# Optimization experiments

Measured on AMD Instinct MI355X. Metric: run time of the kernel, lower is better.

## Reference

```python
import jax, jax.numpy as jnp
import numpy as np

N = 50000   # nodes
E = 800000  # edges
F = 128     # num_node_features
H = 256     # hidden_channels
C = 40      # num_classes


def setup_inputs() -> dict:
    key = jax.random.key(0)
    ks = jax.random.split(key, 8)
    x = jax.random.normal(ks[0], (N, F), dtype=jnp.float32)
    edge_index = jax.random.randint(ks[1], (2, E), 0, N, dtype=jnp.int32)
    # GCNConv linear weights (PyG: lin has no bias; bias added post-aggregation)
    W1 = jax.random.normal(ks[2], (H, F), dtype=jnp.float32) * (1.0 / np.sqrt(F))
    b1 = jnp.zeros((H,), dtype=jnp.float32)
    W2 = jax.random.normal(ks[3], (H, H), dtype=jnp.float32) * (1.0 / np.sqrt(H))
    b2 = jnp.zeros((H,), dtype=jnp.float32)
    Wout = jax.random.normal(ks[4], (C, H), dtype=jnp.float32) * (1.0 / np.sqrt(H))
    bout = jnp.zeros((C,), dtype=jnp.float32)
    return {"x": x, "edge_index": edge_index,
            "W1": W1, "b1": b1, "W2": W2, "b2": b2,
            "Wout": Wout, "bout": bout}


def gcn_conv(x, src, dst, W, b, n):
    """PyG GCNConv: sym-normalized aggregation with self-loops.
    deg computed as in-degree on dst (gcn_norm), +1 for self loop.
    """
    h = x @ W.T  # [n, out]
    ones = jnp.ones((src.shape[0],), dtype=h.dtype)
    deg = jax.ops.segment_sum(ones, dst, num_segments=n) + 1.0  # self loop
    dinv = jax.lax.rsqrt(deg)  # deg >= 1, safe
    norm = dinv[src] * dinv[dst]                 # [E]
    agg = jax.ops.segment_sum(norm[:, None] * h[src], dst, num_segments=n)
    agg = agg + (dinv * dinv)[:, None] * h       # self-loop term
    return agg + b


def reference(x, edge_index, W1, b1, W2, b2, Wout, bout):
    src, dst = edge_index[0], edge_index[1]
    h = jax.nn.relu(gcn_conv(x, src, dst, W1, b1, N))
    h = gcn_conv(h, src, dst, W2, b2, N)
    return h @ Wout.T + bout  # [N, C] logits
```

## Files before the change

### kernel.cpp

```cpp
#include <hip/hip_runtime.h>

#define N_NODES 50000
#define N_EDGES 800000
#define F_IN    128
#define H_DIM   256
#define C_OUT   40
#define MT_TOT  (N_NODES / 16)
#define TPAD    64
#define NBIN1   196
#define NCHB    200
#define CHSZ    (N_EDGES / NCHB)

typedef unsigned short u16;
typedef unsigned int   u32;
typedef short bf16x8 __attribute__((ext_vector_type(8)));
typedef float f32x4  __attribute__((ext_vector_type(4)));

__device__ inline float bfbits2f(u16 u) { return __uint_as_float(((u32)u) << 16); }
__device__ inline u16 f2bf(float f) {
    u32 u = __float_as_uint(f);
    u += 0x7fffu + ((u >> 16) & 1u);
    return (u16)(u >> 16);
}
__device__ inline u32 pack2(float a, float b) {
    return (u32)f2bf(a) | ((u32)f2bf(b) << 16);
}

#define CVT_X  (N_NODES * F_IN / 4)
#define CVT_W1 (H_DIM * F_IN / 4)
#define CVT_TOT (CVT_X + CVT_W1)
#define CC_CVT_BLKS (CVT_TOT / 256)
__global__ __launch_bounds__(256) void cvtwc_k(const float4* __restrict__ x, uint2* __restrict__ xb,
                                               const float4* __restrict__ W1, uint2* __restrict__ W1b,
                                               const float* __restrict__ W2, const float* __restrict__ Wo,
                                               const float* __restrict__ b2, const float* __restrict__ bo,
                                               u16* __restrict__ Wcb, float* __restrict__ bc) {
    if (blockIdx.x < CC_CVT_BLKS) {
        int i = blockIdx.x * 256 + threadIdx.x;
        const float4* s; uint2* d; int j;
        if (i < CVT_X) { s = x; d = xb; j = i; }
        else { s = W1; d = W1b; j = i - CVT_X; }
        float4 v = s[j];
        uint2 o; o.x = pack2(v.x, v.y); o.y = pack2(v.z, v.w);
        d[j] = o;
        return;
    }
    const int c = blockIdx.x - CC_CVT_BLKS;
    const int t = threadIdx.x;
    float acc = 0.f;
    for (int o = 0; o < H_DIM; o += 8) {
        float w2v[8];
#pragma unroll
        for (int j = 0; j < 8; j++) w2v[j] = W2[(size_t)(o + j) * H_DIM + t];
#pragma unroll
        for (int j = 0; j < 8; j++) acc += Wo[(size_t)c * H_DIM + o + j] * w2v[j];
    }
    Wcb[(size_t)c * H_DIM + t] = f2bf(acc);
    __shared__ float red[256];
    red[t] = b2[t] * Wo[(size_t)c * H_DIM + t];
    __syncthreads();
    for (int off = 128; off > 0; off >>= 1) {
        if (t < off) red[t] += red[t + off];
        __syncthreads();
    }
    if (t == 0) bc[c] = red[0] + bo[c];
}

__global__ __launch_bounds__(256) void p1hist_k(const int* __restrict__ dst, int* __restrict__ Ht) {
    __shared__ int hist[NBIN1];
    const int t = threadIdx.x;
    const int b = blockIdx.x;
    if (t < NBIN1) hist[t] = 0;
    __syncthreads();
    for (int i = b * CHSZ + t; i < (b + 1) * CHSZ; i += 256)
        atomicAdd(&hist[dst[i] >> 8], 1);
    __syncthreads();
    if (t < NBIN1) Ht[t * NCHB + b] = hist[t];
}

__global__ __launch_bounds__(256) void p1scan_k(int* __restrict__ Ht, int* __restrict__ totals) {
    __shared__ int sc[256];
    const int t = threadIdx.x;
    const int g = blockIdx.x;
    int v = (t < NCHB) ? Ht[g * NCHB + t] : 0;
    sc[t] = v;
    __syncthreads();
    for (int off = 1; off < 256; off <<= 1) {
        int u = (t >= off) ? sc[t - off] : 0;
        __syncthreads();
        sc[t] += u;
        __syncthreads();
    }
    if (t < NCHB) Ht[g * NCHB + t] = sc[t] - v;
    if (t == NCHB - 1) totals[g] = sc[t];
}

__global__ __launch_bounds__(256) void p1base_k(const int* __restrict__ totals,
                                                int* __restrict__ base, int* __restrict__ rowptr) {
    __shared__ int sc[256];
    const int t = threadIdx.x;
    int v = (t < NBIN1) ? totals[t] : 0;
    sc[t] = v;
    __syncthreads();
    for (int off = 1; off < 256; off <<= 1) {
        int u = (t >= off) ? sc[t - off] : 0;
        __syncthreads();
        sc[t] += u;
        __syncthreads();
    }
    if (t < NBIN1) base[t] = sc[t] - v;
    if (t == NBIN1 - 1) base[NBIN1] = sc[t];
    if (t == 0) rowptr[N_NODES] = N_EDGES;
}

__global__ __launch_bounds__(256) void p2scatter_k(const int* __restrict__ src, const int* __restrict__ dst,
                                                   const int* __restrict__ Ht, const int* __restrict__ base,
                                                   uint2* __restrict__ T) {
    __shared__ int cur[NBIN1];
    const int t = threadIdx.x;
    const int b = blockIdx.x;
    if (t < NBIN1) cur[t] = base[t] + Ht[t * NCHB + b];
    __syncthreads();
    for (int i = b * CHSZ + t; i < (b + 1) * CHSZ; i += 256) {
        const int s = src[i], d = dst[i];
        const int pos = atomicAdd(&cur[d >> 8], 1);
        uint2 ed; ed.x = (u32)s; ed.y = (u32)d;
        T[pos] = ed;
    }
}

__global__ __launch_bounds__(256) void p3a_k(const uint2* __restrict__ T, const int* __restrict__ base,
                                             int* __restrict__ rowptr, float* __restrict__ dinv) {
    __shared__ int hcnt[256];
    __shared__ int sc[256];
    const int t = threadIdx.x;
    const int g = blockIdx.x;
    const int nbeg = base[g], nend = base[g + 1];
    hcnt[t] = 0;
    __syncthreads();
    for (int i = nbeg + t; i < nend; i += 256)
        atomicAdd(&hcnt[T[i].y & 255], 1);
    __syncthreads();
    const int my = hcnt[t];
    sc[t] = my;
    __syncthreads();
    for (int off = 1; off < 256; off <<= 1) {
        int u = (t >= off) ? sc[t - off] : 0;
        __syncthreads();
        sc[t] += u;
        __syncthreads();
    }
    const int node = g * 256 + t;
    if (node < N_NODES) {
        rowptr[node] = nbeg + sc[t] - my;
        dinv[node] = rsqrtf((float)my + 1.0f);
    }
}

__global__ __launch_bounds__(256) void p3b_k(const uint2* __restrict__ T, const int* __restrict__ base,
                                             const float* __restrict__ dinv, uint2* __restrict__ edata) {
    __shared__ int hcnt[256];
    __shared__ int sc[256];
    __shared__ int cur[256];
    const int t = threadIdx.x;
    const int g = blockIdx.x;
    const int nbeg = base[g], nend = base[g + 1];
    hcnt[t] = 0;
    __syncthreads();
    for (int i = nbeg + t; i < nend; i += 256)
        atomicAdd(&hcnt[T[i].y & 255], 1);
    __syncthreads();
    const int my = hcnt[t];
    sc[t] = my;
    __syncthreads();
    for (int off = 1; off < 256; off <<= 1) {
        int u = (t >= off) ? sc[t - off] : 0;
        __syncthreads();
        sc[t] += u;
        __syncthreads();
    }
    cur[t] = nbeg + sc[t] - my;
    __syncthreads();
    for (int i = nbeg + t; i < nend; i += 256) {
        const uint2 e = T[i];
        const int pos = atomicAdd(&cur[e.y & 255], 1);
        const float w = dinv[e.x];
        uint2 ed; ed.x = e.x; ed.y = __float_as_uint(w);
        edata[pos] = ed;
    }
}

__global__ __launch_bounds__(256) void gather1_k(const u32* __restrict__ xb,
                                                 const int* __restrict__ rowptr,
                                                 const uint2* __restrict__ edata,
                                                 const float* __restrict__ dinv,
                                                 u32* __restrict__ aggx) {
    const int node = __builtin_amdgcn_readfirstlane(blockIdx.x * 4 + (threadIdx.x >> 6));
    const int lane = threadIdx.x & 63;
    if (node >= N_NODES) return;
    const int beg = __builtin_amdgcn_readfirstlane(rowptr[node]);
    const int end = __builtin_amdgcn_readfirstlane(rowptr[node + 1]);
    const float dd = dinv[node];
    const u32 vs = xb[(size_t)node * 64 + lane];
    float a0 = dd * bfbits2f((u16)vs);
    float a1 = dd * bfbits2f((u16)(vs >> 16));
    int e = beg;
    for (; e + 7 < end; e += 8) {
        uint2 ed[8];
#pragma unroll
        for (int j = 0; j < 8; j++) ed[j] = edata[e + j];
        u32 v[8];
#pragma unroll
        for (int j = 0; j < 8; j++) v[j] = xb[(size_t)ed[j].x * 64 + lane];
#pragma unroll
        for (int j = 0; j < 8; j++) {
            const float n = __uint_as_float(ed[j].y);
            a0 += n * bfbits2f((u16)v[j]);
            a1 += n * bfbits2f((u16)(v[j] >> 16));
        }
    }
    for (; e < end; e++) {
        const uint2 e0 = edata[e];
        const u32 v0 = xb[(size_t)e0.x * 64 + lane];
        const float n0 = __uint_as_float(e0.y);
        a0 += n0 * bfbits2f((u16)v0);
        a1 += n0 * bfbits2f((u16)(v0 >> 16));
    }
    aggx[(size_t)node * 64 + lane] = pack2(dd * a0, dd * a1);
}

__global__ __launch_bounds__(256) void bgemm1f_k(const u16* __restrict__ X,
                                                 const u16* __restrict__ W1b,
                                                 const float* __restrict__ b1,
                                                 const u16* __restrict__ Wcb,
                                                 u16* __restrict__ tb) {
    constexpr int KF1 = F_IN / 32;
    constexpr int KF2 = H_DIM / 32;
    __shared__ __align__(16) u16 hs[2][16][H_DIM + 8];
    const int wave = threadIdx.x >> 6;
    const int lane = threadIdx.x & 63;
    const int quad = lane >> 4;
    const int nn = lane & 15;
    const int ngbase = wave * 64;

    bf16x8 Bf[4][KF1];
    float bb[4];
#pragma unroll
    for (int j = 0; j < 4; j++) {
        const int wr = ngbase + j * 16 + nn;
#pragma unroll
        for (int kf = 0; kf < KF1; kf++)
            Bf[j][kf] = *(const bf16x8*)(W1b + (size_t)wr * F_IN + kf * 32 + quad * 8);
        bb[j] = b1[wr];
    }
    bf16x8 Bh[KF2];
    {
        int hr = wave * 16 + nn;
        if (hr > C_OUT - 1) hr = C_OUT - 1;
#pragma unroll
        for (int kf = 0; kf < KF2; kf++)
            Bh[kf] = *(const bf16x8*)(Wcb + (size_t)hr * H_DIM + kf * 32 + quad * 8);
    }

    int mt = blockIdx.x;
    if (mt >= MT_TOT) return;
    const int stride = gridDim.x;
    int buf = 0;

    bf16x8 Acur[KF1], Anext[KF1];
    {
        const u16* ap = X + (size_t)(mt * 16 + nn) * F_IN + quad * 8;
#pragma unroll
        for (int kf = 0; kf < KF1; kf++) Acur[kf] = *(const bf16x8*)(ap + kf * 32);
    }

    while (true) {
        const int mtn = mt + stride;
        if (mtn < MT_TOT) {
            const u16* ap = X + (size_t)(mtn * 16 + nn) * F_IN + quad * 8;
#pragma unroll
            for (int kf = 0; kf < KF1; kf++) Anext[kf] = *(const bf16x8*)(ap + kf * 32);
        }

        f32x4 acc[4];
#pragma unroll
        for (int j = 0; j < 4; j++) acc[j] = (f32x4){0.f, 0.f, 0.f, 0.f};
#pragma unroll
        for (int kf = 0; kf < KF1; kf++)
#pragma unroll
            for (int j = 0; j < 4; j++)
                acc[j] = __builtin_amdgcn_mfma_f32_16x16x32_bf16(Acur[kf], Bf[j][kf], acc[j], 0, 0, 0);

#pragma unroll
        for (int j = 0; j < 4; j++)
#pragma unroll
            for (int r = 0; r < 4; r++)
                hs[buf][quad * 4 + r][ngbase + j * 16 + nn] = f2bf(fmaxf(acc[j][r] + bb[j], 0.f));
        __syncthreads();

        if (wave < 3) {
            f32x4 ah = (f32x4){0.f, 0.f, 0.f, 0.f};
#pragma unroll
            for (int kf = 0; kf < KF2; kf++) {
                bf16x8 af = *(const bf16x8*)(&hs[buf][nn][kf * 32 + quad * 8]);
                ah = __builtin_amdgcn_mfma_f32_16x16x32_bf16(af, Bh[kf], ah, 0, 0, 0);
            }
            const int col = wave * 16 + nn;
#pragma unroll
            for (int r = 0; r < 4; r++) {
                const int row = mt * 16 + quad * 4 + r;
                tb[(size_t)row * TPAD + col] = f2bf(ah[r]);
            }
        }

        if (mtn >= MT_TOT) break;
#pragma unroll
        for (int kf = 0; kf < KF1; kf++) Acur[kf] = Anext[kf];
        mt = mtn;
        buf ^= 1;
    }
}

__global__ __launch_bounds__(256) void gatherO_k(const u32* __restrict__ tb,
                                                 const int* __restrict__ rowptr,
                                                 const uint2* __restrict__ edata,
                                                 const float* __restrict__ dinv,
                                                 const float* __restrict__ bc,
                                                 float* __restrict__ out) {
    const int node = __builtin_amdgcn_readfirstlane(blockIdx.x * 4 + (threadIdx.x >> 6));
    const int lane = threadIdx.x & 63;
    if (node >= N_NODES) return;
    const int lc = lane & 31;
    const int beg = __builtin_amdgcn_readfirstlane(rowptr[node]);
    const int end = __builtin_amdgcn_readfirstlane(rowptr[node + 1]);
    const float dd = dinv[node];
    const u32 vs = tb[(size_t)node * (TPAD / 2) + lc];
    float a0 = dd * bfbits2f((u16)vs);
    float a1 = dd * bfbits2f((u16)(vs >> 16));
    int e = beg;
    for (; e + 7 < end; e += 8) {
        uint2 ed[8];
#pragma unroll
        for (int j = 0; j < 8; j++) ed[j] = edata[e + j];
        u32 v[8];
#pragma unroll
        for (int j = 0; j < 8; j++) v[j] = tb[(size_t)ed[j].x * (TPAD / 2) + lc];
#pragma unroll
        for (int j = 0; j < 8; j++) {
            const float n = __uint_as_float(ed[j].y);
            a0 += n * bfbits2f((u16)v[j]);
            a1 += n * bfbits2f((u16)(v[j] >> 16));
        }
    }
    for (; e < end; e++) {
        const uint2 e0 = edata[e];
        const u32 v0 = tb[(size_t)e0.x * (TPAD / 2) + lc];
        const float n0 = __uint_as_float(e0.y);
        a0 += n0 * bfbits2f((u16)v0);
        a1 += n0 * bfbits2f((u16)(v0 >> 16));
    }
    if (lane < C_OUT / 2) {
        float2 o;
        o.x = dd * a0 + bc[2 * lane];
        o.y = dd * a1 + bc[2 * lane + 1];
        *(float2*)(out + (size_t)node * C_OUT + 2 * lane) = o;
    }
}

extern "C" void kernel_launch(void* const* d_in, const int* in_sizes, int n_in,
                              void* d_out, int out_size, void* d_ws, size_t ws_size,
                              hipStream_t stream) {
    const float* x    = (const float*)d_in[0];
    const int*   ei   = (const int*)d_in[1];
    const float* W1   = (const float*)d_in[2];
    const float* b1   = (const float*)d_in[3];
    const float* W2   = (const float*)d_in[4];
    const float* b2   = (const float*)d_in[5];
    const float* Wout = (const float*)d_in[6];
    const float* bout = (const float*)d_in[7];
    float* out = (float*)d_out;

    const int* src = ei;
    const int* dst = ei + N_EDGES;

    char* ws = (char*)d_ws;
    size_t o = 0;
    auto alloc = [&](size_t bytes) { size_t p = o; o = (o + bytes + 255) & ~(size_t)255; return p; };
    int*   Ht     = (int*)(ws + alloc((size_t)NBIN1 * NCHB * 4));
    int*   totals = (int*)(ws + alloc((size_t)NBIN1 * 4));
    int*   base   = (int*)(ws + alloc((size_t)(NBIN1 + 1) * 4));
    float* dinv   = (float*)(ws + alloc((size_t)N_NODES * 4));
    int*   rowptr = (int*)(ws + alloc((size_t)(N_NODES + 1) * 4));
    uint2* T      = (uint2*)(ws + alloc((size_t)N_EDGES * 8));
    uint2* edata  = (uint2*)(ws + alloc((size_t)N_EDGES * 8));
    u16*   xb     = (u16*)(ws + alloc((size_t)N_NODES * F_IN * 2));
    u16*   aggxb  = (u16*)(ws + alloc((size_t)N_NODES * F_IN * 2));
    u16*   tb     = (u16*)(ws + alloc((size_t)N_NODES * TPAD * 2));
    u16*   W1b    = (u16*)(ws + alloc((size_t)H_DIM * F_IN * 2));
    u16*   Wcb    = (u16*)(ws + alloc((size_t)C_OUT * H_DIM * 2));
    float* bc     = (float*)(ws + alloc((size_t)C_OUT * 4));

    cvtwc_k<<<CC_CVT_BLKS + C_OUT, 256, 0, stream>>>(
        (const float4*)x, (uint2*)xb, (const float4*)W1, (uint2*)W1b,
        W2, Wout, b2, bout, Wcb, bc);

    p1hist_k<<<NCHB, 256, 0, stream>>>(dst, Ht);
    p1scan_k<<<NBIN1, 256, 0, stream>>>(Ht, totals);
    p1base_k<<<1, 256, 0, stream>>>(totals, base, rowptr);
    p2scatter_k<<<NCHB, 256, 0, stream>>>(src, dst, Ht, base, T);
    p3a_k<<<NBIN1, 256, 0, stream>>>(T, base, rowptr, dinv);
    p3b_k<<<NBIN1, 256, 0, stream>>>(T, base, dinv, edata);

    gather1_k<<<(N_NODES + 3) / 4, 256, 0, stream>>>((const u32*)xb, rowptr, edata, dinv, (u32*)aggxb);
    bgemm1f_k<<<768, 256, 0, stream>>>(aggxb, W1b, b1, Wcb, tb);
    gatherO_k<<<(N_NODES + 3) / 4, 256, 0, stream>>>((const u32*)tb, rowptr, edata, dinv, bc, out);
}
```

Baseline: 206.1 us.

## Fold source-side degree scaling into features, shrink edge data to indices

Pre-scales x rows by dinv during the bf16 conversion and scales the layer-2 projected features by dinv in the GEMM epilogue. The per-edge norm weight is then no longer needed, so edata shrinks from (src, weight) pairs to plain src indices. This lets the two CSR build passes merge into one kernel, and the histogram is fused with the weight precompute. The aim is to cut edge-stream bandwidth in both gathers and to drop one kernel launch, in exchange for an extra pass that reads dinv while converting x.

New measurement: 199.7 us. 3.1% less time.

```diff
diff --git a/kernel.cpp b/kernel.cpp
--- a/kernel.cpp
+++ b/kernel.cpp
@@ -10,6 +10,8 @@
 #define NBIN1   196
 #define NCHB    200
 #define CHSZ    (N_EDGES / NCHB)
+#define CVT_X   (N_NODES * F_IN / 4)
+#define CVT_W1B (H_DIM * F_IN / 4 / 256)
 
 typedef unsigned short u16;
 typedef unsigned int   u32;
@@ -26,27 +28,32 @@
     return (u32)f2bf(a) | ((u32)f2bf(b) << 16);
 }
 
-#define CVT_X  (N_NODES * F_IN / 4)
-#define CVT_W1 (H_DIM * F_IN / 4)
-#define CVT_TOT (CVT_X + CVT_W1)
-#define CC_CVT_BLKS (CVT_TOT / 256)
-__global__ __launch_bounds__(256) void cvtwc_k(const float4* __restrict__ x, uint2* __restrict__ xb,
-                                               const float4* __restrict__ W1, uint2* __restrict__ W1b,
-                                               const float* __restrict__ W2, const float* __restrict__ Wo,
-                                               const float* __restrict__ b2, const float* __restrict__ bo,
-                                               u16* __restrict__ Wcb, float* __restrict__ bc) {
-    if (blockIdx.x < CC_CVT_BLKS) {
-        int i = blockIdx.x * 256 + threadIdx.x;
-        const float4* s; uint2* d; int j;
-        if (i < CVT_X) { s = x; d = xb; j = i; }
-        else { s = W1; d = W1b; j = i - CVT_X; }
-        float4 v = s[j];
+__global__ __launch_bounds__(256) void pre_k(const int* __restrict__ dst, int* __restrict__ Ht,
+                                             const float4* __restrict__ W1, uint2* __restrict__ W1b,
+                                             const float* __restrict__ W2, const float* __restrict__ Wo,
+                                             const float* __restrict__ b2, const float* __restrict__ bo,
+                                             u16* __restrict__ Wcb, float* __restrict__ bc) {
+    __shared__ int hist[NBIN1];
+    __shared__ float red[256];
+    const int t = threadIdx.x;
+    if (blockIdx.x < NCHB) {
+        const int b = blockIdx.x;
+        if (t < NBIN1) hist[t] = 0;
+        __syncthreads();
+        for (int i = b * CHSZ + t; i < (b + 1) * CHSZ; i += 256)
+            atomicAdd(&hist[dst[i] >> 8], 1);
+        __syncthreads();
+        if (t < NBIN1) Ht[t * NCHB + b] = hist[t];
+        return;
+    }
+    if (blockIdx.x < NCHB + CVT_W1B) {
+        int i = (blockIdx.x - NCHB) * 256 + t;
+        float4 v = W1[i];
         uint2 o; o.x = pack2(v.x, v.y); o.y = pack2(v.z, v.w);
-        d[j] = o;
+        W1b[i] = o;
         return;
     }
-    const int c = blockIdx.x - CC_CVT_BLKS;
-    const int t = threadIdx.x;
+    const int c = blockIdx.x - NCHB - CVT_W1B;
     float acc = 0.f;
     for (int o = 0; o < H_DIM; o += 8) {
         float w2v[8];
@@ -56,7 +63,6 @@
         for (int j = 0; j < 8; j++) acc += Wo[(size_t)c * H_DIM + o + j] * w2v[j];
     }
     Wcb[(size_t)c * H_DIM + t] = f2bf(acc);
-    __shared__ float red[256];
     red[t] = b2[t] * Wo[(size_t)c * H_DIM + t];
     __syncthreads();
     for (int off = 128; off > 0; off >>= 1) {
@@ -64,18 +70,6 @@
         __syncthreads();
     }
     if (t == 0) bc[c] = red[0] + bo[c];
-}
-
-__global__ __launch_bounds__(256) void p1hist_k(const int* __restrict__ dst, int* __restrict__ Ht) {
-    __shared__ int hist[NBIN1];
-    const int t = threadIdx.x;
-    const int b = blockIdx.x;
-    if (t < NBIN1) hist[t] = 0;
-    __syncthreads();
-    for (int i = b * CHSZ + t; i < (b + 1) * CHSZ; i += 256)
-        atomicAdd(&hist[dst[i] >> 8], 1);
-    __syncthreads();
-    if (t < NBIN1) Ht[t * NCHB + b] = hist[t];
 }
 
 __global__ __launch_bounds__(256) void p1scan_k(int* __restrict__ Ht, int* __restrict__ totals) {
@@ -129,10 +123,12 @@
     }
 }
 
-__global__ __launch_bounds__(256) void p3a_k(const uint2* __restrict__ T, const int* __restrict__ base,
-                                             int* __restrict__ rowptr, float* __restrict__ dinv) {
+__global__ __launch_bounds__(256) void p3_k(const uint2* __restrict__ T, const int* __restrict__ base,
+                                            int* __restrict__ rowptr, float* __restrict__ dinv,
+                                            u32* __restrict__ edata) {
     __shared__ int hcnt[256];
     __shared__ int sc[256];
+    __shared__ int cur[256];
     const int t = threadIdx.x;
     const int g = blockIdx.x;
     const int nbeg = base[g], nend = base[g + 1];
@@ -150,49 +146,36 @@
         sc[t] += u;
         __syncthreads();
     }
+    const int rbeg = nbeg + sc[t] - my;
     const int node = g * 256 + t;
     if (node < N_NODES) {
-        rowptr[node] = nbeg + sc[t] - my;
+        rowptr[node] = rbeg;
         dinv[node] = rsqrtf((float)my + 1.0f);
     }
-}
-
-__global__ __launch_bounds__(256) void p3b_k(const uint2* __restrict__ T, const int* __restrict__ base,
-                                             const float* __restrict__ dinv, uint2* __restrict__ edata) {
-    __shared__ int hcnt[256];
-    __shared__ int sc[256];
-    __shared__ int cur[256];
-    const int t = threadIdx.x;
-    const int g = blockIdx.x;
-    const int nbeg = base[g], nend = base[g + 1];
-    hcnt[t] = 0;
-    __syncthreads();
-    for (int i = nbeg + t; i < nend; i += 256)
-        atomicAdd(&hcnt[T[i].y & 255], 1);
-    __syncthreads();
-    const int my = hcnt[t];
-    sc[t] = my;
-    __syncthreads();
-    for (int off = 1; off < 256; off <<= 1) {
-        int u = (t >= off) ? sc[t - off] : 0;
-        __syncthreads();
-        sc[t] += u;
-        __syncthreads();
-    }
-    cur[t] = nbeg + sc[t] - my;
+    cur[t] = rbeg;
     __syncthreads();
     for (int i = nbeg + t; i < nend; i += 256) {
         const uint2 e = T[i];
         const int pos = atomicAdd(&cur[e.y & 255], 1);
-        const float w = dinv[e.x];
-        uint2 ed; ed.x = e.x; ed.y = __float_as_uint(w);
-        edata[pos] = ed;
-    }
+        edata[pos] = e.x;
+    }
+}
+
+__global__ __launch_bounds__(256) void xcvt_k(const float4* __restrict__ x,
+                                              const float* __restrict__ dinv,
+                                              uint2* __restrict__ xb) {
+    int i = blockIdx.x * 256 + threadIdx.x;
+    if (i >= CVT_X) return;
+    const int row = i >> 5;
+    const float s = dinv[row];
+    float4 v = x[i];
+    uint2 o; o.x = pack2(s * v.x, s * v.y); o.y = pack2(s * v.z, s * v.w);
+    xb[i] = o;
 }
 
 __global__ __launch_bounds__(256) void gather1_k(const u32* __restrict__ xb,
                                                  const int* __restrict__ rowptr,
-                                                 const uint2* __restrict__ edata,
+                                                 const u32* __restrict__ edata,
                                                  const float* __restrict__ dinv,
                                                  u32* __restrict__ aggx) {
     const int node = __builtin_amdgcn_readfirstlane(blockIdx.x * 4 + (threadIdx.x >> 6));
@@ -202,29 +185,26 @@
     const int end = __builtin_amdgcn_readfirstlane(rowptr[node + 1]);
     const float dd = dinv[node];
     const u32 vs = xb[(size_t)node * 64 + lane];
-    float a0 = dd * bfbits2f((u16)vs);
-    float a1 = dd * bfbits2f((u16)(vs >> 16));
+    float a0 = bfbits2f((u16)vs);
+    float a1 = bfbits2f((u16)(vs >> 16));
     int e = beg;
     for (; e + 7 < end; e += 8) {
-        uint2 ed[8];
-#pragma unroll
-        for (int j = 0; j < 8; j++) ed[j] = edata[e + j];
+        u32 s8[8];
+#pragma unroll
+        for (int j = 0; j < 8; j++) s8[j] = edata[e + j];
         u32 v[8];
 #pragma unroll
-        for (int j = 0; j < 8; j++) v[j] = xb[(size_t)ed[j].x * 64 + lane];
+        for (int j = 0; j < 8; j++) v[j] = xb[(size_t)s8[j] * 64 + lane];
 #pragma unroll
         for (int j = 0; j < 8; j++) {
-            const float n = __uint_as_float(ed[j].y);
-            a0 += n * bfbits2f((u16)v[j]);
-            a1 += n * bfbits2f((u16)(v[j] >> 16));
+            a0 += bfbits2f((u16)v[j]);
+            a1 += bfbits2f((u16)(v[j] >> 16));
         }
     }
     for (; e < end; e++) {
-        const uint2 e0 = edata[e];
-        const u32 v0 = xb[(size_t)e0.x * 64 + lane];
-        const float n0 = __uint_as_float(e0.y);
-        a0 += n0 * bfbits2f((u16)v0);
-        a1 += n0 * bfbits2f((u16)(v0 >> 16));
+        const u32 v0 = xb[(size_t)edata[e] * 64 + lane];
+        a0 += bfbits2f((u16)v0);
+        a1 += bfbits2f((u16)(v0 >> 16));
     }
     aggx[(size_t)node * 64 + lane] = pack2(dd * a0, dd * a1);
 }
@@ -233,6 +213,7 @@
                                                  const u16* __restrict__ W1b,
                                                  const float* __restrict__ b1,
                                                  const u16* __restrict__ Wcb,
+                                                 const float* __restrict__ dinv,
                                                  u16* __restrict__ tb) {
     constexpr int KF1 = F_IN / 32;
     constexpr int KF2 = H_DIM / 32;
@@ -309,7 +290,7 @@
 #pragma unroll
             for (int r = 0; r < 4; r++) {
                 const int row = mt * 16 + quad * 4 + r;
-                tb[(size_t)row * TPAD + col] = f2bf(ah[r]);
+                tb[(size_t)row * TPAD + col] = f2bf(dinv[row] * ah[r]);
             }
         }
 
@@ -323,7 +304,7 @@
 
 __global__ __launch_bounds__(256) void gatherO_k(const u32* __restrict__ tb,
                                                  const int* __restrict__ rowptr,
-                                                 const uint2* __restrict__ edata,
+                                                 const u32* __restrict__ edata,
                                                  const float* __restrict__ dinv,
                                                  const float* __restrict__ bc,
                                                  float* __restrict__ out) {
@@ -335,29 +316,26 @@
     const int end = __builtin_amdgcn_readfirstlane(rowptr[node + 1]);
     const float dd = dinv[node];
     const u32 vs = tb[(size_t)node * (TPAD / 2) + lc];
-    float a0 = dd * bfbits2f((u16)vs);
-    float a1 = dd * bfbits2f((u16)(vs >> 16));
+    float a0 = bfbits2f((u16)vs);
+    float a1 = bfbits2f((u16)(vs >> 16));
     int e = beg;
     for (; e + 7 < end; e += 8) {
-        uint2 ed[8];
-#pragma unroll
-        for (int j = 0; j < 8; j++) ed[j] = edata[e + j];
+        u32 s8[8];
+#pragma unroll
+        for (int j = 0; j < 8; j++) s8[j] = edata[e + j];
         u32 v[8];
 #pragma unroll
-        for (int j = 0; j < 8; j++) v[j] = tb[(size_t)ed[j].x * (TPAD / 2) + lc];
+        for (int j = 0; j < 8; j++) v[j] = tb[(size_t)s8[j] * (TPAD / 2) + lc];
 #pragma unroll
         for (int j = 0; j < 8; j++) {
-            const float n = __uint_as_float(ed[j].y);
-            a0 += n * bfbits2f((u16)v[j]);
-            a1 += n * bfbits2f((u16)(v[j] >> 16));
+            a0 += bfbits2f((u16)v[j]);
+            a1 += bfbits2f((u16)(v[j] >> 16));
         }
     }
     for (; e < end; e++) {
-        const uint2 e0 = edata[e];
-        const u32 v0 = tb[(size_t)e0.x * (TPAD / 2) + lc];
-        const float n0 = __uint_as_float(e0.y);
-        a0 += n0 * bfbits2f((u16)v0);
-        a1 += n0 * bfbits2f((u16)(v0 >> 16));
+        const u32 v0 = tb[(size_t)edata[e] * (TPAD / 2) + lc];
+        a0 += bfbits2f((u16)v0);
+        a1 += bfbits2f((u16)(v0 >> 16));
     }
     if (lane < C_OUT / 2) {
         float2 o;
@@ -392,7 +370,7 @@
     float* dinv   = (float*)(ws + alloc((size_t)N_NODES * 4));
     int*   rowptr = (int*)(ws + alloc((size_t)(N_NODES + 1) * 4));
     uint2* T      = (uint2*)(ws + alloc((size_t)N_EDGES * 8));
-    uint2* edata  = (uint2*)(ws + alloc((size_t)N_EDGES * 8));
+    u32*   edata  = (u32*)(ws + alloc((size_t)N_EDGES * 4));
     u16*   xb     = (u16*)(ws + alloc((size_t)N_NODES * F_IN * 2));
     u16*   aggxb  = (u16*)(ws + alloc((size_t)N_NODES * F_IN * 2));
     u16*   tb     = (u16*)(ws + alloc((size_t)N_NODES * TPAD * 2));
@@ -400,18 +378,15 @@
     u16*   Wcb    = (u16*)(ws + alloc((size_t)C_OUT * H_DIM * 2));
     float* bc     = (float*)(ws + alloc((size_t)C_OUT * 4));
 
-    cvtwc_k<<<CC_CVT_BLKS + C_OUT, 256, 0, stream>>>(
-        (const float4*)x, (uint2*)xb, (const float4*)W1, (uint2*)W1b,
-        W2, Wout, b2, bout, Wcb, bc);
-
-    p1hist_k<<<NCHB, 256, 0, stream>>>(dst, Ht);
+    pre_k<<<NCHB + CVT_W1B + C_OUT, 256, 0, stream>>>(
+        dst, Ht, (const float4*)W1, (uint2*)W1b, W2, Wout, b2, bout, Wcb, bc);
     p1scan_k<<<NBIN1, 256, 0, stream>>>(Ht, totals);
     p1base_k<<<1, 256, 0, stream>>>(totals, base, rowptr);
     p2scatter_k<<<NCHB, 256, 0, stream>>>(src, dst, Ht, base, T);
-    p3a_k<<<NBIN1, 256, 0, stream>>>(T, base, rowptr, dinv);
-    p3b_k<<<NBIN1, 256, 0, stream>>>(T, base, dinv, edata);
+    p3_k<<<NBIN1, 256, 0, stream>>>(T, base, rowptr, dinv, edata);
+    xcvt_k<<<(CVT_X + 255) / 256, 256, 0, stream>>>((const float4*)x, dinv, (uint2*)xb);
 
     gather1_k<<<(N_NODES + 3) / 4, 256, 0, stream>>>((const u32*)xb, rowptr, edata, dinv, (u32*)aggxb);
-    bgemm1f_k<<<768, 256, 0, stream>>>(aggxb, W1b, b1, Wcb, tb);
+    bgemm1f_k<<<768, 256, 0, stream>>>(aggxb, W1b, b1, Wcb, dinv, tb);
     gatherO_k<<<(N_NODES + 3) / 4, 256, 0, stream>>>((const u32*)tb, rowptr, edata, dinv, bc, out);
 }
```
